# Kernel optimization log

Measured on AMD Instinct MI355X. Metric: run time of the kernel, lower is better.

The kernel has to match this reference:

```python
import jax, jax.numpy as jnp
import numpy as np

T = 0.2          # temperature
W = 0.1          # loss weight
BIG = 2 ** 30    # sentinel label for masked-out samples


def setup_inputs() -> dict:
    key = jax.random.key(0)
    k1, k2, k3, k4 = jax.random.split(key, 4)
    bs, C, Gn, S = 32, 128, 256, 16
    grouped_features = jax.random.normal(k1, (bs, C, Gn, S), dtype=jnp.float32)
    # instance labels in [-1, 8): -1 = background
    proposal_instance_mask = jax.random.randint(k2, (bs, Gn, S), -1, 8, dtype=jnp.int32)
    # seed indices with duplicates possible (range 40 over 16 samples)
    grouped_indices = jax.random.randint(k3, (bs, Gn, S), 0, 40, dtype=jnp.int32)
    context_compen = jax.random.normal(k4, (1, C), dtype=jnp.float32)
    return {
        "proposal_instance_mask": proposal_instance_mask,
        "grouped_features": grouped_features,
        "grouped_indices": grouped_indices,
        "context_compen": context_compen,
    }


def _group_loss(feat, idx, lab, ctx):
    # feat: [S, C], idx: [S], lab: [S], ctx: [C]
    # NOTE: sum_{a,b} f_a . g_b / (n_f * n_g) == mean(f) . mean(g), so the
    # original tiny-mm contrastive loss reduces to pairwise dots of per-instance means.
    S, C = feat.shape
    pos = jnp.arange(S)
    # unique count of seed indices -> truncate to first u samples (as in torch code)
    si = jnp.sort(idx)
    u = 1 + jnp.sum(si[1:] != si[:-1])
    valid = pos < u
    lab_m = jnp.where(valid, lab, BIG)
    # per-group unique labels (sorted), jit-friendly
    sl = jnp.sort(lab_m)
    new = jnp.concatenate([jnp.ones((1,), bool), sl[1:] != sl[:-1]])
    cid = jnp.cumsum(new) - 1                      # compact id of each sorted label
    uniq = jnp.full((S,), BIG, sl.dtype).at[cid].set(sl)
    n_labels = jnp.sum(new & (sl != BIG))          # number of distinct valid labels
    has_bg = uniq[0] == -1                         # -1 sorts first if present
    # per-instance mean features via segment scatter-add
    comp = jnp.searchsorted(uniq, lab_m)           # sample -> compact instance slot
    sums = jnp.zeros((S, C), feat.dtype).at[comp].add(jnp.where(valid[:, None], feat, 0.0))
    cnts = jnp.zeros((S,), feat.dtype).at[comp].add(valid.astype(feat.dtype))
    means = sums / jnp.maximum(cnts, 1.0)[:, None]
    hb = has_bg.astype(jnp.int32)
    fg_count = n_labels - hb
    inst_num = fg_count + 1                        # bg slot always present
    # row 0 = bg mean (or context_compen if no bg), rows 1.. = fg means
    gidx = jnp.clip(pos + hb - 1, 0, S - 1)
    M = means[gidx]
    M = M.at[0].set(jnp.where(has_bg, M[0], ctx))
    inst_valid = pos < inst_num
    sim = (M @ M.T) / T                            # [S, S] tiny matmul of means
    sim_m = jnp.where(inst_valid[None, :], sim, -jnp.inf)
    lse = jax.scipy.special.logsumexp(sim_m, axis=1)
    li = lse - jnp.diagonal(sim)                   # -log(pos/(pos+neg)) per fg row
    fg_mask = inst_valid & (pos >= 1)
    gl = jnp.sum(jnp.where(fg_mask, li, 0.0)) / jnp.maximum(inst_num - 1, 1).astype(feat.dtype)
    return gl, fg_count >= 1


def reference(proposal_instance_mask, grouped_features, grouped_indices, context_compen):
    bs, C, Gn, S = grouped_features.shape
    feats = grouped_features.transpose(0, 2, 3, 1).reshape(-1, S, C)  # [G, S, C]
    idxs = grouped_indices.reshape(-1, S)
    labs = proposal_instance_mask.reshape(-1, S)
    ctx = context_compen[0]
    gl, gv = jax.vmap(lambda f, i, l: _group_loss(f, i, l, ctx))(feats, idxs, labs)
    gvf = gv.astype(gl.dtype)
    return jnp.sum(gl * gvf) / jnp.sum(gvf) * W
```

## Files before the change

### kernel.cpp

```cpp
#include <hip/hip_runtime.h>

#define GQ    8192
#define BLKG  8
#define NBLK  (GQ / BLKG)
#define MROW  132
#define STG   (64 * MROW)
#define SIMW  72
#define SQRT5 2.23606797749978969f

__global__ __launch_bounds__(64 * BLKG, 8) void group_loss_kernel(
    const int*   __restrict__ labs,
    const float* __restrict__ feats,
    const int*   __restrict__ idxs,
    const float* __restrict__ ctx,
    float2*      __restrict__ ws)
{
    __shared__ float SH[STG + BLKG * SIMW + 2 * BLKG];

    const int l  = threadIdx.x & 63;
    const int w  = threadIdx.x >> 6;
    const int g0 = blockIdx.x * BLKG;
    const int g  = g0 + w;
    const int b  = g0 >> 8;
    const int gn0 = g0 & 255;
    float* SIM  = SH + STG + w * SIMW;
    float* PART = SH + STG + BLKG * SIMW;

    const float* base = feats + (long)b * 524288 + (long)gn0 * 16;
    const int lo = l & 31;

    int myidx = -1, mylab = -2;
    if (l < 16) { myidx = idxs[g * 16 + l]; mylab = labs[g * 16 + l]; }
    const float cx0 = ctx[l], cx1 = ctx[l + 64];

    #pragma unroll
    for (int k = 0; k < 4; ++k) {
        const int ch = w * 8 + k * 2 + (l >> 5);
        const float4 v = *(const float4*)(base + (long)ch * 4096 + lo * 4);
        *(float4*)(SH + ch * MROW + lo * 4) = v;
    }

    unsigned long long mm = ~0ull;
    #pragma unroll
    for (int bit = 0; bit < 6; ++bit) {
        const unsigned long long bb = __ballot((myidx >> bit) & 1);
        mm &= ((myidx >> bit) & 1) ? bb : ~bb;
    }
    const bool dup = (mm & ((1ull << l) - 1) & 0xFFFFull) != 0ull;
    const int u = __popcll(__ballot((l < 16) && !dup));

    const bool valid = l < u;
    const int bid = valid ? (mylab + 1) : 255;

    int cnt9[9];
    #pragma unroll
    for (int r = 0; r < 9; ++r) cnt9[r] = __popcll(__ballot(bid == r));
    const bool has_bg = cnt9[0] > 0;
    int fg_count = 0, pm = 0;
    #pragma unroll
    for (int r = 1; r < 9; ++r)
        if (cnt9[r] > 0) { ++fg_count; pm |= 1 << r; }

    float m0[9] = {0,0,0,0,0,0,0,0,0};
    float m1[9] = {0,0,0,0,0,0,0,0,0};

    __syncthreads();
    {
        const float* R = SH + l * MROW + w * 16;
        #pragma unroll
        for (int q = 0; q < 4; ++q) {
            const float4 x = *(const float4*)(R + 4 * q);
            #pragma unroll
            for (int e = 0; e < 4; ++e) {
                const int s = 4 * q + e;
                if (s < u) {
                    const int bs = __builtin_amdgcn_readlane(bid, s);
                    const float v = (e == 0) ? x.x : (e == 1) ? x.y
                                  : (e == 2) ? x.z : x.w;
                    switch (bs) {
                        case 0: m0[0] += v; break;  case 1: m0[1] += v; break;
                        case 2: m0[2] += v; break;  case 3: m0[3] += v; break;
                        case 4: m0[4] += v; break;  case 5: m0[5] += v; break;
                        case 6: m0[6] += v; break;  case 7: m0[7] += v; break;
                        case 8: m0[8] += v; break;
                    }
                }
            }
        }
    }
    __syncthreads();

    #pragma unroll
    for (int k = 0; k < 4; ++k) {
        const int ch = w * 8 + k * 2 + (l >> 5);
        const float4 v = *(const float4*)(base + (long)(64 + ch) * 4096 + lo * 4);
        *(float4*)(SH + ch * MROW + lo * 4) = v;
    }
    __syncthreads();

    {
        const float* R = SH + l * MROW + w * 16;
        #pragma unroll
        for (int q = 0; q < 4; ++q) {
            const float4 x = *(const float4*)(R + 4 * q);
            #pragma unroll
            for (int e = 0; e < 4; ++e) {
                const int s = 4 * q + e;
                if (s < u) {
                    const int bs = __builtin_amdgcn_readlane(bid, s);
                    const float v = (e == 0) ? x.x : (e == 1) ? x.y
                                  : (e == 2) ? x.z : x.w;
                    switch (bs) {
                        case 0: m1[0] += v; break;  case 1: m1[1] += v; break;
                        case 2: m1[2] += v; break;  case 3: m1[3] += v; break;
                        case 4: m1[4] += v; break;  case 5: m1[5] += v; break;
                        case 6: m1[6] += v; break;  case 7: m1[7] += v; break;
                        case 8: m1[8] += v; break;
                    }
                }
            }
        }
    }

    #pragma unroll
    for (int r = 0; r < 9; ++r) {
        const float sc = SQRT5 / (float)(cnt9[r] > 0 ? cnt9[r] : 1);
        m0[r] *= sc; m1[r] *= sc;
    }
    if (!has_bg) { m0[0] = cx0 * SQRT5; m1[0] = cx1 * SQRT5; }

    #pragma unroll
    for (int r = 1; r <= 8; ++r) {
        float p[8];
        #pragma unroll
        for (int j = 0; j < 8; ++j)
            p[j] = m0[r] * m0[j] + m1[r] * m1[j];
        #pragma unroll
        for (int i = 0; i < 4; ++i) {
            const float send = (l & 32) ? p[i] : p[i + 4];
            const float recv = __shfl_xor(send, 32);
            p[i] = ((l & 32) ? p[i + 4] : p[i]) + recv;
        }
        #pragma unroll
        for (int i = 0; i < 2; ++i) {
            const float send = (l & 16) ? p[i] : p[i + 2];
            const float recv = __shfl_xor(send, 16);
            p[i] = ((l & 16) ? p[i + 2] : p[i]) + recv;
        }
        {
            const float send = (l & 8) ? p[0] : p[1];
            const float recv = __shfl_xor(send, 8);
            p[0] = ((l & 8) ? p[1] : p[0]) + recv;
        }
        p[0] += __shfl_xor(p[0], 4);
        p[0] += __shfl_xor(p[0], 2);
        p[0] += __shfl_xor(p[0], 1);
        if ((l & 7) == 0) SIM[(r - 1) * 8 + (l >> 3)] = p[0];
    }
    float s88 = m0[8] * m0[8] + m1[8] * m1[8];
    s88 += __shfl_xor(s88, 1);  s88 += __shfl_xor(s88, 2);
    s88 += __shfl_xor(s88, 4);  s88 += __shfl_xor(s88, 8);
    s88 += __shfl_xor(s88, 16); s88 += __shfl_xor(s88, 32);

    const int cm = pm | 1;
    const float NINF = __int_as_float(0xFF800000);
    float li = 0.0f;
    if (l >= 1 && l <= 8) {
        const float* Rw = SIM + (l - 1) * 8;
        const float4 ra = *(const float4*)(Rw);
        const float4 rb = *(const float4*)(Rw + 4);
        const float s8 = SIM[56 + l];
        float srow[9] = { ra.x, ra.y, ra.z, ra.w, rb.x, rb.y, rb.z, rb.w,
                          (l == 8) ? s88 : s8 };
        float vmax = NINF, diag = 0.0f, v[9];
        #pragma unroll
        for (int j = 0; j < 9; ++j) {
            v[j] = ((cm >> j) & 1) ? srow[j] : NINF;
            vmax = fmaxf(vmax, v[j]);
            if (j >= 1) diag = (l == j) ? srow[j] : diag;
        }
        float se = 0.0f;
        #pragma unroll
        for (int j = 0; j < 9; ++j) se += __expf(v[j] - vmax);
        li = vmax + __logf(se) - diag;
        li = ((pm >> l) & 1) ? li : 0.0f;
    }

    float ssum = li;
    ssum += __shfl_down(ssum, 8);
    ssum += __shfl_down(ssum, 4);
    ssum += __shfl_down(ssum, 2);
    ssum += __shfl_down(ssum, 1);

    if (l == 0) {
        PART[2 * w]     = ssum / (float)(fg_count > 0 ? fg_count : 1);
        PART[2 * w + 1] = (fg_count > 0) ? 1.0f : 0.0f;
    }
    __syncthreads();
    if (threadIdx.x == 0) {
        float px = 0.0f, py = 0.0f;
        #pragma unroll
        for (int i = 0; i < BLKG; ++i) { px += PART[2 * i]; py += PART[2 * i + 1]; }
        ws[blockIdx.x] = make_float2(px, py);
    }
}

__global__ __launch_bounds__(256) void reduce_kernel(
    const float2* __restrict__ ws, float* __restrict__ out)
{
    __shared__ float sa[256], sb[256];
    const int t = threadIdx.x;
    float a = 0.0f, b2 = 0.0f;
    #pragma unroll
    for (int i = 0; i < NBLK / 256; ++i) {
        const float2 v = ws[t + i * 256];
        a += v.x; b2 += v.y;
    }
    sa[t] = a; sb[t] = b2;
    __syncthreads();
    for (int off = 128; off > 0; off >>= 1) {
        if (t < off) { sa[t] += sa[t + off]; sb[t] += sb[t + off]; }
        __syncthreads();
    }
    if (t == 0) out[0] = 0.1f * (sa[0] / sb[0]);
}

extern "C" void kernel_launch(void* const* d_in, const int* in_sizes, int n_in,
                              void* d_out, int out_size, void* d_ws, size_t ws_size,
                              hipStream_t stream) {
    const int*   labs  = (const int*)d_in[0];
    const float* feats = (const float*)d_in[1];
    const int*   idxs  = (const int*)d_in[2];
    const float* ctx   = (const float*)d_in[3];
    float* out = (float*)d_out;
    float2* ws = (float2*)d_ws;

    group_loss_kernel<<<NBLK, 64 * BLKG, 0, stream>>>(labs, feats, idxs, ctx, ws);
    reduce_kernel<<<1, 256, 0, stream>>>(ws, out);
}
```

Measured before the change: 108.7 us.

## Issue both feature-half loads up front and read second half directly per lane

Both halves of the feature tile are now loaded into registers at the start. The first half still goes through LDS for the transpose, while the second half is read directly with one lane per channel and 16 contiguous floats, so it skips shared memory altogether. Two of the three block barriers and the serialized second global-load phase go away, and the two label-dispatch loops merge into one pass. The cost is higher register pressure, which may reduce occupancy, and the direct loads use a strided per-lane access pattern that coalesces less well.

```diff
diff --git a/kernel.cpp b/kernel.cpp
--- a/kernel.cpp
+++ b/kernel.cpp
@@ -33,12 +33,17 @@
     if (l < 16) { myidx = idxs[g * 16 + l]; mylab = labs[g * 16 + l]; }
     const float cx0 = ctx[l], cx1 = ctx[l + 64];
 
+    float4 areg[4];
     #pragma unroll
     for (int k = 0; k < 4; ++k) {
         const int ch = w * 8 + k * 2 + (l >> 5);
-        const float4 v = *(const float4*)(base + (long)ch * 4096 + lo * 4);
-        *(float4*)(SH + ch * MROW + lo * 4) = v;
-    }
+        areg[k] = *(const float4*)(base + (long)ch * 4096 + lo * 4);
+    }
+    const float* bptr = feats + (long)b * 524288 + (long)(l + 64) * 4096
+                              + (long)(gn0 + w) * 16;
+    float4 breg[4];
+    #pragma unroll
+    for (int k = 0; k < 4; ++k) breg[k] = *(const float4*)(bptr + 4 * k);
 
     unsigned long long mm = ~0ull;
     #pragma unroll
@@ -61,63 +66,41 @@
     for (int r = 1; r < 9; ++r)
         if (cnt9[r] > 0) { ++fg_count; pm |= 1 << r; }
 
+    #pragma unroll
+    for (int k = 0; k < 4; ++k) {
+        const int ch = w * 8 + k * 2 + (l >> 5);
+        *(float4*)(SH + ch * MROW + lo * 4) = areg[k];
+    }
+    __syncthreads();
+
+    float fa[16], fb[16];
+    {
+        const float* R = SH + l * MROW + w * 16;
+        #pragma unroll
+        for (int q = 0; q < 4; ++q) {
+            const float4 x = *(const float4*)(R + 4 * q);
+            fa[4*q+0] = x.x; fa[4*q+1] = x.y; fa[4*q+2] = x.z; fa[4*q+3] = x.w;
+            fb[4*q+0] = breg[q].x; fb[4*q+1] = breg[q].y;
+            fb[4*q+2] = breg[q].z; fb[4*q+3] = breg[q].w;
+        }
+    }
+
     float m0[9] = {0,0,0,0,0,0,0,0,0};
     float m1[9] = {0,0,0,0,0,0,0,0,0};
-
-    __syncthreads();
-    {
-        const float* R = SH + l * MROW + w * 16;
-        #pragma unroll
-        for (int q = 0; q < 4; ++q) {
-            const float4 x = *(const float4*)(R + 4 * q);
-            #pragma unroll
-            for (int e = 0; e < 4; ++e) {
-                const int s = 4 * q + e;
-                if (s < u) {
-                    const int bs = __builtin_amdgcn_readlane(bid, s);
-                    const float v = (e == 0) ? x.x : (e == 1) ? x.y
-                                  : (e == 2) ? x.z : x.w;
-                    switch (bs) {
-                        case 0: m0[0] += v; break;  case 1: m0[1] += v; break;
-                        case 2: m0[2] += v; break;  case 3: m0[3] += v; break;
-                        case 4: m0[4] += v; break;  case 5: m0[5] += v; break;
-                        case 6: m0[6] += v; break;  case 7: m0[7] += v; break;
-                        case 8: m0[8] += v; break;
-                    }
-                }
-            }
-        }
-    }
-    __syncthreads();
-
-    #pragma unroll
-    for (int k = 0; k < 4; ++k) {
-        const int ch = w * 8 + k * 2 + (l >> 5);
-        const float4 v = *(const float4*)(base + (long)(64 + ch) * 4096 + lo * 4);
-        *(float4*)(SH + ch * MROW + lo * 4) = v;
-    }
-    __syncthreads();
-
-    {
-        const float* R = SH + l * MROW + w * 16;
-        #pragma unroll
-        for (int q = 0; q < 4; ++q) {
-            const float4 x = *(const float4*)(R + 4 * q);
-            #pragma unroll
-            for (int e = 0; e < 4; ++e) {
-                const int s = 4 * q + e;
-                if (s < u) {
-                    const int bs = __builtin_amdgcn_readlane(bid, s);
-                    const float v = (e == 0) ? x.x : (e == 1) ? x.y
-                                  : (e == 2) ? x.z : x.w;
-                    switch (bs) {
-                        case 0: m1[0] += v; break;  case 1: m1[1] += v; break;
-                        case 2: m1[2] += v; break;  case 3: m1[3] += v; break;
-                        case 4: m1[4] += v; break;  case 5: m1[5] += v; break;
-                        case 6: m1[6] += v; break;  case 7: m1[7] += v; break;
-                        case 8: m1[8] += v; break;
-                    }
-                }
+    #pragma unroll
+    for (int s = 0; s < 16; ++s) {
+        if (s < u) {
+            const int bs = __builtin_amdgcn_readlane(bid, s);
+            switch (bs) {
+                case 0: m0[0] += fa[s]; m1[0] += fb[s]; break;
+                case 1: m0[1] += fa[s]; m1[1] += fb[s]; break;
+                case 2: m0[2] += fa[s]; m1[2] += fb[s]; break;
+                case 3: m0[3] += fa[s]; m1[3] += fb[s]; break;
+                case 4: m0[4] += fa[s]; m1[4] += fb[s]; break;
+                case 5: m0[5] += fa[s]; m1[5] += fb[s]; break;
+                case 6: m0[6] += fa[s]; m1[6] += fb[s]; break;
+                case 7: m0[7] += fa[s]; m1[7] += fb[s]; break;
+                case 8: m0[8] += fa[s]; m1[8] += fb[s]; break;
             }
         }
     }
```

Measured after the change: 119.9 us. 10.3% more time.
